# Kernel tuning notes

Hardware: AMD Instinct MI355X
Metric: run time of the kernel (lower is better)

Reference implementation:

```python
import jax, jax.numpy as jnp
import numpy as np

N_NODES = 100000
N_EDGES = 1600000
IN_DIM, HID, OUT_DIM = 256, 128, 64


def _glorot(key, shape):
    lim = float(np.sqrt(6.0 / (shape[0] + shape[1])))
    return jax.random.uniform(key, shape, jnp.float32, -lim, lim)


def setup_inputs() -> dict:
    key = jax.random.key(0)
    ks = jax.random.split(key, 8)
    x = jax.random.normal(ks[0], (N_NODES, IN_DIM), jnp.float32)
    edge_index = jax.random.randint(ks[1], (2, N_EDGES), 0, N_NODES, jnp.int64)
    return {
        "x": x,
        "edge_index": edge_index,
        "W1": _glorot(ks[2], (IN_DIM, HID)),
        "b1": jnp.zeros((HID,), jnp.float32),
        "W2": _glorot(ks[3], (HID, HID)),
        "b2": jnp.zeros((HID,), jnp.float32),
        "Wf1": _glorot(ks[4], (HID, HID)),
        "bf1": jnp.zeros((HID,), jnp.float32),
        "Wf2": _glorot(ks[5], (HID, OUT_DIM)),
        "bf2": jnp.zeros((OUT_DIM,), jnp.float32),
    }


def _gcn_conv(x, src, dst, W, b):
    # x: [N, Fin]; src/dst: [E+N] (self-loops already appended)
    n = x.shape[0]
    deg = jax.ops.segment_sum(jnp.ones_like(dst, dtype=x.dtype), dst, num_segments=n)
    dinv = jnp.where(deg > 0, jax.lax.rsqrt(deg), 0.0)
    norm = dinv[src] * dinv[dst]                      # [E+N]
    h = x @ W                                         # [N, Fout] transform first (PyG order)
    msg = h[src] * norm[:, None]                      # gather + scale
    return jax.ops.segment_sum(msg, dst, num_segments=n) + b


def reference(x, edge_index, W1, b1, W2, b2, Wf1, bf1, Wf2, bf2):
    n = x.shape[0]
    loops = jnp.arange(n, dtype=edge_index.dtype)
    src = jnp.concatenate([edge_index[0], loops])
    dst = jnp.concatenate([edge_index[1], loops])
    h = jax.nn.relu(_gcn_conv(x, src, dst, W1, b1))
    h = jax.nn.relu(_gcn_conv(h, src, dst, W2, b2))
    h = jax.nn.relu(h @ Wf1 + bf1)
    return h @ Wf2 + bf2
```

## Files before the change

kernel.cpp:

```cpp
#include <hip/hip_runtime.h>
#include <hip/hip_fp16.h>


typedef __attribute__((ext_vector_type(8))) short short8;
typedef __attribute__((ext_vector_type(4))) float f32x4;

constexpr int SLOT = 48;
constexpr int NBUK = 128;
constexpr int BCAP = 16000;
constexpr int NPB  = 782;

static __device__ __forceinline__ unsigned short f2bf(float f) {
    unsigned u = __float_as_uint(f);
    unsigned r = (u + 0x7fff + ((u >> 16) & 1)) >> 16;
    return (unsigned short)r;
}
static __device__ __forceinline__ float bf2f(unsigned short h) {
    return __uint_as_float(((unsigned)h) << 16);
}

static __device__ __forceinline__ void pack_one(
    const float* __restrict__ W, unsigned short* __restrict__ P,
    int Kd, int Nd, int idx)
{
    int k = idx / Nd, nn = idx % Nd;
    float w = W[idx];
    unsigned short hi = f2bf(w);
    unsigned short lo = f2bf(w - bf2f(hi));
    int k0 = k >> 5, kin = k & 31, bk = kin >> 3, i = kin & 7;
    int lane = (nn & 15) + (bk << 4);
    int cn = nn >> 4, NF = Nd >> 4;
    size_t base = (size_t)(k0 * NF + cn) * 1024;
    P[base + lane * 8 + i] = hi;
    P[base + 512 + lane * 8 + i] = lo;
}

__global__ void pack_all_k(const float* __restrict__ W1, const float* __restrict__ W2,
                           const float* __restrict__ Wf1, const float* __restrict__ Wf2,
                           unsigned short* __restrict__ W1p, unsigned short* __restrict__ W2p,
                           unsigned short* __restrict__ Wf1p, unsigned short* __restrict__ Wf2p,
                           int* __restrict__ gcur) {
    int gid = blockIdx.x * blockDim.x + threadIdx.x;
    const int n1 = 256 * 128, n2 = n1 + 128 * 128, n3 = n2 + 128 * 128, n4 = n3 + 128 * 64;
    if      (gid < n1) pack_one(W1,  W1p,  256, 128, gid);
    else if (gid < n2) pack_one(W2,  W2p,  128, 128, gid - n1);
    else if (gid < n3) pack_one(Wf1, Wf1p, 128, 128, gid - n2);
    else if (gid < n4) pack_one(Wf2, Wf2p, 128, 64,  gid - n3);
    else if (gid < n4 + NBUK) gcur[gid - n4] = 0;
}

template<int K, int N, bool SCALE, bool BIAS, bool RELU, bool HOUT>
static __device__ __forceinline__ void gemm_body(
    const float* __restrict__ A, const unsigned short* __restrict__ Bp,
    const float* __restrict__ bias, const float* __restrict__ dinv,
    void* __restrict__ Cv, int M, int bid)
{
    constexpr int NF = N / 16;
    constexpr int KS = K / 32;
    const int tid  = threadIdx.x;
    const int lane = tid & 63;
    const int wid  = tid >> 6;
    const int m16  = lane & 15;
    const int kg   = lane >> 4;
    const int rowB = bid * 128 + wid * 32;

    f32x4 acc[2][NF];
#pragma unroll
    for (int rm = 0; rm < 2; ++rm)
#pragma unroll
        for (int cn = 0; cn < NF; ++cn)
            acc[rm][cn] = (f32x4){0.f, 0.f, 0.f, 0.f};

    const short8* bp8 = (const short8*)Bp;

    for (int ks = 0; ks < KS; ++ks) {
        short8 ahi[2], alo[2];
#pragma unroll
        for (int rm = 0; rm < 2; ++rm) {
            int r = rowB + rm * 16 + m16;
            if (r >= M) r = M - 1;
            const float* ap = A + (size_t)r * K + ks * 32 + kg * 8;
            float4 a0 = *(const float4*)ap;
            float4 a1 = *(const float4*)(ap + 4);
            float av[8] = {a0.x, a0.y, a0.z, a0.w, a1.x, a1.y, a1.z, a1.w};
#pragma unroll
            for (int i = 0; i < 8; ++i) {
                unsigned short h = f2bf(av[i]);
                ahi[rm][i] = (short)h;
                alo[rm][i] = (short)f2bf(av[i] - bf2f(h));
            }
        }
#pragma unroll
        for (int cn = 0; cn < NF; ++cn) {
            size_t fb = (size_t)(ks * NF + cn) * 128 + lane;
            short8 bhi = bp8[fb];
            short8 blo = bp8[fb + 64];
#pragma unroll
            for (int rm = 0; rm < 2; ++rm) {
                acc[rm][cn] = __builtin_amdgcn_mfma_f32_16x16x32_bf16(ahi[rm], bhi, acc[rm][cn], 0, 0, 0);
                acc[rm][cn] = __builtin_amdgcn_mfma_f32_16x16x32_bf16(ahi[rm], blo, acc[rm][cn], 0, 0, 0);
                acc[rm][cn] = __builtin_amdgcn_mfma_f32_16x16x32_bf16(alo[rm], bhi, acc[rm][cn], 0, 0, 0);
            }
        }
    }
#pragma unroll
    for (int rm = 0; rm < 2; ++rm) {
#pragma unroll
        for (int r = 0; r < 4; ++r) {
            int row = rowB + rm * 16 + kg * 4 + r;
            if (row < M) {
                float sc = SCALE ? dinv[row] : 1.f;
#pragma unroll
                for (int cn = 0; cn < NF; ++cn) {
                    float v = acc[rm][cn][r];
                    if (SCALE) v *= sc;
                    if (BIAS)  v += bias[cn * 16 + m16];
                    if (RELU)  v = fmaxf(v, 0.f);
                    if (HOUT)
                        ((__half*)Cv)[(size_t)row * N + cn * 16 + m16] = __float2half(v);
                    else
                        ((float*)Cv)[(size_t)row * N + cn * 16 + m16] = v;
                }
            }
        }
    }
}

template<int K, int N, bool SCALE, bool BIAS, bool RELU, bool HOUT>
__global__ __launch_bounds__(256) void mgemm_k(
    const float* __restrict__ A, const unsigned short* __restrict__ Bp,
    const float* __restrict__ bias, const float* __restrict__ dinv,
    void* __restrict__ Cv, int M)
{
    gemm_body<K, N, SCALE, BIAS, RELU, HOUT>(A, Bp, bias, dinv, Cv, M, blockIdx.x);
}

__global__ __launch_bounds__(256) void mega1_k(
    const float* __restrict__ x, const unsigned short* __restrict__ W1p,
    __half* __restrict__ bufH, int M,
    const int* __restrict__ esrc, const int* __restrict__ edst,
    int2* __restrict__ bins, int* __restrict__ gcur, int E, int nGemm, int nChunk)
{
    __shared__ int hist[NBUK];
    __shared__ int bpos[NBUK];
    if ((int)blockIdx.x < nGemm) {
        gemm_body<256, 128, false, false, false, true>(x, W1p, nullptr, nullptr, bufH, M, blockIdx.x);
        return;
    }
    const int nb = gridDim.x - nGemm;
    for (int c = blockIdx.x - nGemm; c < nChunk; c += nb) {
        int base = c * 1024;
        if (threadIdx.x < NBUK) hist[threadIdx.x] = 0;
        __syncthreads();
        int d[4], s[4], bk[4], pl[4], ok[4];
#pragma unroll
        for (int i = 0; i < 4; ++i) {
            int e = base + threadIdx.x + i * 256;
            ok[i] = (e < E);
            d[i]  = ok[i] ? edst[e] : 0;
            s[i]  = ok[i] ? esrc[e] : 0;
            bk[i] = (int)((unsigned)d[i] / (unsigned)NPB);
        }
#pragma unroll
        for (int i = 0; i < 4; ++i)
            if (ok[i]) pl[i] = atomicAdd(&hist[bk[i]], 1);
        __syncthreads();
        if (threadIdx.x < NBUK) {
            int h = hist[threadIdx.x];
            bpos[threadIdx.x] = h ? atomicAdd(&gcur[threadIdx.x], h) : 0;
        }
        __syncthreads();
#pragma unroll
        for (int i = 0; i < 4; ++i)
            if (ok[i]) {
                int p = bpos[bk[i]] + pl[i];
                if (p < BCAP) bins[(size_t)bk[i] * BCAP + p] = make_int2(s[i], d[i]);
            }
        __syncthreads();
    }
}

__global__ __launch_bounds__(1024) void fill2_k(
    const int2* __restrict__ bins, const int* __restrict__ gcur,
    int* __restrict__ slot, float* __restrict__ dinv, int n)
{
    const int b = blockIdx.x;
    const int base = b * NPB;
    const int nn = min(NPB, n - base);
    if (nn <= 0) return;
    __shared__ int cnt[NPB];
    for (int i = threadIdx.x; i < nn; i += 1024) cnt[i] = 0;
    __syncthreads();
    int ec = gcur[b]; if (ec > BCAP) ec = BCAP;
    for (int i = threadIdx.x; i < ec; i += 1024) {
        int2 e = bins[(size_t)b * BCAP + i];
        int li = e.y - base;
        int p = atomicAdd(&cnt[li], 1);
        if (p < SLOT - 1) slot[(size_t)e.y * SLOT + 1 + p] = e.x;
    }
    __syncthreads();
    for (int i = threadIdx.x; i < nn; i += 1024) {
        int c = cnt[i];
        slot[(size_t)(base + i) * SLOT] = c;
        dinv[base + i] = 1.0f / sqrtf((float)(c + 1));
    }
}

struct alignas(16) H8 { __half2 h[4]; };

template<bool SS>
__global__ __launch_bounds__(256) void agg_k(
    const H8* __restrict__ hs, const int* __restrict__ slot,
    const float* __restrict__ dinv, const float* __restrict__ bias,
    float* __restrict__ out, int n)
{
    int t    = blockIdx.x * blockDim.x + threadIdx.x;
    int node = t >> 4;
    int ln   = threadIdx.x & 15;
    if (node >= n) return;
    const int* row = slot + (size_t)node * SLOT;
    int cnt = row[0]; if (cnt > SLOT - 1) cnt = SLOT - 1;
    float dn = dinv[node];

    float acc[8];
    {
        H8 v = hs[(size_t)node * 16 + ln];
        float sf = SS ? dn : 1.f;
#pragma unroll
        for (int q = 0; q < 4; ++q) {
            float2 f = __half22float2(v.h[q]);
            acc[q * 2] = f.x * sf; acc[q * 2 + 1] = f.y * sf;
        }
    }
    int j = 0;
    for (; j + 4 <= cnt; j += 4) {
        int s0 = row[1 + j], s1 = row[2 + j], s2 = row[3 + j], s3 = row[4 + j];
        float w0 = 1.f, w1 = 1.f, w2 = 1.f, w3 = 1.f;
        if (SS) { w0 = dinv[s0]; w1 = dinv[s1]; w2 = dinv[s2]; w3 = dinv[s3]; }
        H8 v0 = hs[(size_t)s0 * 16 + ln];
        H8 v1 = hs[(size_t)s1 * 16 + ln];
        H8 v2 = hs[(size_t)s2 * 16 + ln];
        H8 v3 = hs[(size_t)s3 * 16 + ln];
#pragma unroll
        for (int q = 0; q < 4; ++q) {
            float2 f0 = __half22float2(v0.h[q]);
            float2 f1 = __half22float2(v1.h[q]);
            float2 f2 = __half22float2(v2.h[q]);
            float2 f3 = __half22float2(v3.h[q]);
            if (SS) {
                acc[q*2]   = fmaf(w0, f0.x, fmaf(w1, f1.x, fmaf(w2, f2.x, fmaf(w3, f3.x, acc[q*2]))));
                acc[q*2+1] = fmaf(w0, f0.y, fmaf(w1, f1.y, fmaf(w2, f2.y, fmaf(w3, f3.y, acc[q*2+1]))));
            } else {
                acc[q*2]     += (f0.x + f1.x) + (f2.x + f3.x);
                acc[q*2 + 1] += (f0.y + f1.y) + (f2.y + f3.y);
            }
        }
    }
    for (; j < cnt; ++j) {
        int s = row[1 + j];
        float w = SS ? dinv[s] : 1.f;
        H8 v = hs[(size_t)s * 16 + ln];
#pragma unroll
        for (int q = 0; q < 4; ++q) {
            float2 f = __half22float2(v.h[q]);
            acc[q*2]     = fmaf(w, f.x, acc[q*2]);
            acc[q*2 + 1] = fmaf(w, f.y, acc[q*2 + 1]);
        }
    }
    float4 b0 = ((const float4*)bias)[ln * 2];
    float4 b1 = ((const float4*)bias)[ln * 2 + 1];
    float4 r0, r1;
    r0.x = fmaxf(fmaf(acc[0], dn, b0.x), 0.f);
    r0.y = fmaxf(fmaf(acc[1], dn, b0.y), 0.f);
    r0.z = fmaxf(fmaf(acc[2], dn, b0.z), 0.f);
    r0.w = fmaxf(fmaf(acc[3], dn, b0.w), 0.f);
    r1.x = fmaxf(fmaf(acc[4], dn, b1.x), 0.f);
    r1.y = fmaxf(fmaf(acc[5], dn, b1.y), 0.f);
    r1.z = fmaxf(fmaf(acc[6], dn, b1.z), 0.f);
    r1.w = fmaxf(fmaf(acc[7], dn, b1.w), 0.f);
    float4* op = (float4*)out;
    op[(size_t)node * 32 + ln * 2]     = r0;
    op[(size_t)node * 32 + ln * 2 + 1] = r1;
}

extern "C" void kernel_launch(void* const* d_in, const int* in_sizes, int n_in,
                              void* d_out, int out_size, void* d_ws, size_t ws_size,
                              hipStream_t stream) {
    const float* x    = (const float*)d_in[0];
    const int*   eidx = (const int*)d_in[1];
    const float* W1   = (const float*)d_in[2];
    const float* b1   = (const float*)d_in[3];
    const float* W2   = (const float*)d_in[4];
    const float* b2   = (const float*)d_in[5];
    const float* Wf1  = (const float*)d_in[6];
    const float* bf1  = (const float*)d_in[7];
    const float* Wf2  = (const float*)d_in[8];
    const float* bf2  = (const float*)d_in[9];
    float* out = (float*)d_out;

    const int IN = 256, HID = 128;
    const int n = in_sizes[0] / IN;
    const int E = in_sizes[1] / 2;
    const int* esrc = eidx;
    const int* edst = eidx + E;

    char* ws = (char*)d_ws;
    float*  bufB = (float*) (ws);
    int2*   bins = (int2*)  (ws);
    __half* bufH = (__half*)(ws + 51200000);
    int*    slot = (int*)   (ws + 76800000);
    float*  dinv = (float*) (ws + 96000000);
    int*    gcur = (int*)   (ws + 96400000);
    unsigned short* W1p  = (unsigned short*)(ws + 96500000);
    unsigned short* W2p  = (unsigned short*)(ws + 96631072);
    unsigned short* Wf1p = (unsigned short*)(ws + 96696608);
    unsigned short* Wf2p = (unsigned short*)(ws + 96762144);

    const int TB = 256;
    const int nPack  = 256*128 + 128*128 + 128*128 + 128*64 + NBUK;
    const int gGemm  = (n + 127) / 128;
    const int nChunk = (E + 1023) / 1024;
    const int gBin   = 384;
    const int gAgg   = (n * 16 + TB - 1) / TB;

    pack_all_k<<<(nPack + TB - 1) / TB, TB, 0, stream>>>(W1, W2, Wf1, Wf2,
                                                          W1p, W2p, Wf1p, Wf2p, gcur);
    mega1_k<<<gGemm + gBin, TB, 0, stream>>>(x, W1p, bufH, n, esrc, edst,
                                             bins, gcur, E, gGemm, nChunk);
    fill2_k<<<NBUK, 1024, 0, stream>>>(bins, gcur, slot, dinv, n);
    agg_k<true><<<gAgg, TB, 0, stream>>>((const H8*)bufH, slot, dinv, b1, bufB, n);
    mgemm_k<128, 128, true,  false, false, true ><<<gGemm, TB, 0, stream>>>(bufB, W2p, nullptr, dinv, bufH, n);
    agg_k<false><<<gAgg, TB, 0, stream>>>((const H8*)bufH, slot, dinv, b2, bufB, n);
    mgemm_k<128, 128, false, true,  true,  false><<<gGemm, TB, 0, stream>>>(bufB, Wf1p, bf1, nullptr, bufB, n);
    mgemm_k<128, 64,  false, true,  false, false><<<gGemm, TB, 0, stream>>>(bufB, Wf2p, bf2, nullptr, out, n);
}
```

Baseline: 446.2 us.

## Store intermediate activations in fp16 and restructure edge binning to one chunk per block

Aggregation outputs and the MLP intermediate activations are now stored as fp16 instead of fp32, and the GEMMs read half-precision A operands through a templated loader. This roughly halves the memory traffic between the aggregate and GEMM stages. The edge binning now uses 256 buckets with one 2048-edge chunk per block instead of a persistent grid-stride loop, and bin blocks are placed before the GEMM blocks in the fused launch. The cost is extra fp16 rounding on hidden activations, plus a different overlap between binning and the first GEMM.

```diff
diff --git a/kernel.cpp b/kernel.cpp
--- a/kernel.cpp
+++ b/kernel.cpp
@@ -5,10 +5,14 @@
 typedef __attribute__((ext_vector_type(8))) short short8;
 typedef __attribute__((ext_vector_type(4))) float f32x4;
 
-constexpr int SLOT = 48;
-constexpr int NBUK = 128;
-constexpr int BCAP = 16000;
-constexpr int NPB  = 782;
+constexpr int SLOT   = 48;
+constexpr int NBUK   = 256;
+constexpr int BCAP   = 8000;
+constexpr int NPB    = 391;
+constexpr int ECHUNK = 2048;
+constexpr int EPT    = 8;
+
+struct alignas(16) H8 { __half2 h[4]; };
 
 static __device__ __forceinline__ unsigned short f2bf(float f) {
     unsigned u = __float_as_uint(f);
@@ -17,6 +21,21 @@
 }
 static __device__ __forceinline__ float bf2f(unsigned short h) {
     return __uint_as_float(((unsigned)h) << 16);
+}
+
+static __device__ __forceinline__ void loadA8(const float* __restrict__ ap, float* av) {
+    float4 a0 = *(const float4*)ap;
+    float4 a1 = *(const float4*)(ap + 4);
+    av[0] = a0.x; av[1] = a0.y; av[2] = a0.z; av[3] = a0.w;
+    av[4] = a1.x; av[5] = a1.y; av[6] = a1.z; av[7] = a1.w;
+}
+static __device__ __forceinline__ void loadA8(const __half* __restrict__ ap, float* av) {
+    H8 hv = *(const H8*)ap;
+#pragma unroll
+    for (int q = 0; q < 4; ++q) {
+        float2 f = __half22float2(hv.h[q]);
+        av[2 * q] = f.x; av[2 * q + 1] = f.y;
+    }
 }
 
 static __device__ __forceinline__ void pack_one(
@@ -49,9 +68,9 @@
     else if (gid < n4 + NBUK) gcur[gid - n4] = 0;
 }
 
-template<int K, int N, bool SCALE, bool BIAS, bool RELU, bool HOUT>
+template<typename AT, int K, int N, bool SCALE, bool BIAS, bool RELU, bool HOUT>
 static __device__ __forceinline__ void gemm_body(
-    const float* __restrict__ A, const unsigned short* __restrict__ Bp,
+    const AT* __restrict__ A, const unsigned short* __restrict__ Bp,
     const float* __restrict__ bias, const float* __restrict__ dinv,
     void* __restrict__ Cv, int M, int bid)
 {
@@ -79,10 +98,8 @@
         for (int rm = 0; rm < 2; ++rm) {
             int r = rowB + rm * 16 + m16;
             if (r >= M) r = M - 1;
-            const float* ap = A + (size_t)r * K + ks * 32 + kg * 8;
-            float4 a0 = *(const float4*)ap;
-            float4 a1 = *(const float4*)(ap + 4);
-            float av[8] = {a0.x, a0.y, a0.z, a0.w, a1.x, a1.y, a1.z, a1.w};
+            float av[8];
+            loadA8(A + (size_t)r * K + ks * 32 + kg * 8, av);
 #pragma unroll
             for (int i = 0; i < 8; ++i) {
                 unsigned short h = f2bf(av[i]);
@@ -126,58 +143,55 @@
     }
 }
 
-template<int K, int N, bool SCALE, bool BIAS, bool RELU, bool HOUT>
+template<typename AT, int K, int N, bool SCALE, bool BIAS, bool RELU, bool HOUT>
 __global__ __launch_bounds__(256) void mgemm_k(
-    const float* __restrict__ A, const unsigned short* __restrict__ Bp,
+    const AT* __restrict__ A, const unsigned short* __restrict__ Bp,
     const float* __restrict__ bias, const float* __restrict__ dinv,
     void* __restrict__ Cv, int M)
 {
-    gemm_body<K, N, SCALE, BIAS, RELU, HOUT>(A, Bp, bias, dinv, Cv, M, blockIdx.x);
+    gemm_body<AT, K, N, SCALE, BIAS, RELU, HOUT>(A, Bp, bias, dinv, Cv, M, blockIdx.x);
 }
 
 __global__ __launch_bounds__(256) void mega1_k(
     const float* __restrict__ x, const unsigned short* __restrict__ W1p,
     __half* __restrict__ bufH, int M,
     const int* __restrict__ esrc, const int* __restrict__ edst,
-    int2* __restrict__ bins, int* __restrict__ gcur, int E, int nGemm, int nChunk)
+    int2* __restrict__ bins, int* __restrict__ gcur, int E, int nBin)
 {
     __shared__ int hist[NBUK];
     __shared__ int bpos[NBUK];
-    if ((int)blockIdx.x < nGemm) {
-        gemm_body<256, 128, false, false, false, true>(x, W1p, nullptr, nullptr, bufH, M, blockIdx.x);
+    if ((int)blockIdx.x >= nBin) {
+        gemm_body<float, 256, 128, false, false, false, true>(
+            x, W1p, nullptr, nullptr, bufH, M, blockIdx.x - nBin);
         return;
     }
-    const int nb = gridDim.x - nGemm;
-    for (int c = blockIdx.x - nGemm; c < nChunk; c += nb) {
-        int base = c * 1024;
-        if (threadIdx.x < NBUK) hist[threadIdx.x] = 0;
-        __syncthreads();
-        int d[4], s[4], bk[4], pl[4], ok[4];
-#pragma unroll
-        for (int i = 0; i < 4; ++i) {
-            int e = base + threadIdx.x + i * 256;
-            ok[i] = (e < E);
-            d[i]  = ok[i] ? edst[e] : 0;
-            s[i]  = ok[i] ? esrc[e] : 0;
-            bk[i] = (int)((unsigned)d[i] / (unsigned)NPB);
-        }
-#pragma unroll
-        for (int i = 0; i < 4; ++i)
-            if (ok[i]) pl[i] = atomicAdd(&hist[bk[i]], 1);
-        __syncthreads();
-        if (threadIdx.x < NBUK) {
-            int h = hist[threadIdx.x];
-            bpos[threadIdx.x] = h ? atomicAdd(&gcur[threadIdx.x], h) : 0;
-        }
-        __syncthreads();
-#pragma unroll
-        for (int i = 0; i < 4; ++i)
-            if (ok[i]) {
-                int p = bpos[bk[i]] + pl[i];
-                if (p < BCAP) bins[(size_t)bk[i] * BCAP + p] = make_int2(s[i], d[i]);
-            }
-        __syncthreads();
-    }
+    const int base = blockIdx.x * ECHUNK;
+    hist[threadIdx.x] = 0;
+    __syncthreads();
+    int d[EPT], s[EPT], bk[EPT], pl[EPT], ok[EPT];
+#pragma unroll
+    for (int i = 0; i < EPT; ++i) {
+        int e = base + threadIdx.x + i * 256;
+        ok[i] = (e < E);
+        d[i]  = ok[i] ? edst[e] : 0;
+        s[i]  = ok[i] ? esrc[e] : 0;
+        bk[i] = (int)((unsigned)d[i] / (unsigned)NPB);
+    }
+#pragma unroll
+    for (int i = 0; i < EPT; ++i)
+        if (ok[i]) pl[i] = atomicAdd(&hist[bk[i]], 1);
+    __syncthreads();
+    {
+        int h = hist[threadIdx.x];
+        bpos[threadIdx.x] = h ? atomicAdd(&gcur[threadIdx.x], h) : 0;
+    }
+    __syncthreads();
+#pragma unroll
+    for (int i = 0; i < EPT; ++i)
+        if (ok[i]) {
+            int p = bpos[bk[i]] + pl[i];
+            if (p < BCAP) bins[(size_t)bk[i] * BCAP + p] = make_int2(s[i], d[i]);
+        }
 }
 
 __global__ __launch_bounds__(1024) void fill2_k(
@@ -206,13 +220,11 @@
     }
 }
 
-struct alignas(16) H8 { __half2 h[4]; };
-
 template<bool SS>
 __global__ __launch_bounds__(256) void agg_k(
     const H8* __restrict__ hs, const int* __restrict__ slot,
     const float* __restrict__ dinv, const float* __restrict__ bias,
-    float* __restrict__ out, int n)
+    H8* __restrict__ out, int n)
 {
     int t    = blockIdx.x * blockDim.x + threadIdx.x;
     int node = t >> 4;
@@ -269,18 +281,16 @@
     }
     float4 b0 = ((const float4*)bias)[ln * 2];
     float4 b1 = ((const float4*)bias)[ln * 2 + 1];
-    float4 r0, r1;
-    r0.x = fmaxf(fmaf(acc[0], dn, b0.x), 0.f);
-    r0.y = fmaxf(fmaf(acc[1], dn, b0.y), 0.f);
-    r0.z = fmaxf(fmaf(acc[2], dn, b0.z), 0.f);
-    r0.w = fmaxf(fmaf(acc[3], dn, b0.w), 0.f);
-    r1.x = fmaxf(fmaf(acc[4], dn, b1.x), 0.f);
-    r1.y = fmaxf(fmaf(acc[5], dn, b1.y), 0.f);
-    r1.z = fmaxf(fmaf(acc[6], dn, b1.z), 0.f);
-    r1.w = fmaxf(fmaf(acc[7], dn, b1.w), 0.f);
-    float4* op = (float4*)out;
-    op[(size_t)node * 32 + ln * 2]     = r0;
-    op[(size_t)node * 32 + ln * 2 + 1] = r1;
+    H8 r;
+    r.h[0] = __floats2half2_rn(fmaxf(fmaf(acc[0], dn, b0.x), 0.f),
+                               fmaxf(fmaf(acc[1], dn, b0.y), 0.f));
+    r.h[1] = __floats2half2_rn(fmaxf(fmaf(acc[2], dn, b0.z), 0.f),
+                               fmaxf(fmaf(acc[3], dn, b0.w), 0.f));
+    r.h[2] = __floats2half2_rn(fmaxf(fmaf(acc[4], dn, b1.x), 0.f),
+                               fmaxf(fmaf(acc[5], dn, b1.y), 0.f));
+    r.h[3] = __floats2half2_rn(fmaxf(fmaf(acc[6], dn, b1.z), 0.f),
+                               fmaxf(fmaf(acc[7], dn, b1.w), 0.f));
+    out[(size_t)node * 16 + ln] = r;
 }
 
 extern "C" void kernel_launch(void* const* d_in, const int* in_sizes, int n_in,
@@ -305,32 +315,34 @@
     const int* edst = eidx + E;
 
     char* ws = (char*)d_ws;
-    float*  bufB = (float*) (ws);
-    int2*   bins = (int2*)  (ws);
-    __half* bufH = (__half*)(ws + 51200000);
-    int*    slot = (int*)   (ws + 76800000);
-    float*  dinv = (float*) (ws + 96000000);
-    int*    gcur = (int*)   (ws + 96400000);
-    unsigned short* W1p  = (unsigned short*)(ws + 96500000);
-    unsigned short* W2p  = (unsigned short*)(ws + 96631072);
-    unsigned short* Wf1p = (unsigned short*)(ws + 96696608);
-    unsigned short* Wf2p = (unsigned short*)(ws + 96762144);
+    __half* bufH1 = (__half*)(ws);
+    __half* bufH2 = (__half*)(ws + 25600000);
+    int2*   bins  = (int2*)  (ws + 25600000);
+    int*    slot  = (int*)   (ws + 51200000);
+    float*  dinv  = (float*) (ws + 70400000);
+    int*    gcur  = (int*)   (ws + 70800000);
+    unsigned short* W1p  = (unsigned short*)(ws + 70900000);
+    unsigned short* W2p  = (unsigned short*)(ws + 71040000);
+    unsigned short* Wf1p = (unsigned short*)(ws + 71110000);
+    unsigned short* Wf2p = (unsigned short*)(ws + 71180000);
 
     const int TB = 256;
-    const int nPack  = 256*128 + 128*128 + 128*128 + 128*64 + NBUK;
-    const int gGemm  = (n + 127) / 128;
-    const int nChunk = (E + 1023) / 1024;
-    const int gBin   = 384;
-    const int gAgg   = (n * 16 + TB - 1) / TB;
+    const int nPack = 256*128 + 128*128 + 128*128 + 128*64 + NBUK;
+    const int gGemm = (n + 127) / 128;
+    const int nBin  = (E + ECHUNK - 1) / ECHUNK;
+    const int gAgg  = (n * 16 + TB - 1) / TB;
 
     pack_all_k<<<(nPack + TB - 1) / TB, TB, 0, stream>>>(W1, W2, Wf1, Wf2,
                                                           W1p, W2p, Wf1p, Wf2p, gcur);
-    mega1_k<<<gGemm + gBin, TB, 0, stream>>>(x, W1p, bufH, n, esrc, edst,
-                                             bins, gcur, E, gGemm, nChunk);
+    mega1_k<<<nBin + gGemm, TB, 0, stream>>>(x, W1p, bufH1, n, esrc, edst,
+                                             bins, gcur, E, nBin);
     fill2_k<<<NBUK, 1024, 0, stream>>>(bins, gcur, slot, dinv, n);
-    agg_k<true><<<gAgg, TB, 0, stream>>>((const H8*)bufH, slot, dinv, b1, bufB, n);
-    mgemm_k<128, 128, true,  false, false, true ><<<gGemm, TB, 0, stream>>>(bufB, W2p, nullptr, dinv, bufH, n);
-    agg_k<false><<<gAgg, TB, 0, stream>>>((const H8*)bufH, slot, dinv, b2, bufB, n);
-    mgemm_k<128, 128, false, true,  true,  false><<<gGemm, TB, 0, stream>>>(bufB, Wf1p, bf1, nullptr, bufB, n);
-    mgemm_k<128, 64,  false, true,  false, false><<<gGemm, TB, 0, stream>>>(bufB, Wf2p, bf2, nullptr, out, n);
-}
+    agg_k<true><<<gAgg, TB, 0, stream>>>((const H8*)bufH1, slot, dinv, b1, (H8*)bufH2, n);
+    mgemm_k<__half, 128, 128, true,  false, false, true ><<<gGemm, TB, 0, stream>>>(
+        (const __half*)bufH2, W2p, nullptr, dinv, bufH1, n);
+    agg_k<false><<<gAgg, TB, 0, stream>>>((const H8*)bufH1, slot, dinv, b2, (H8*)bufH2, n);
+    mgemm_k<__half, 128, 128, false, true,  true,  true ><<<gGemm, TB, 0, stream>>>(
+        (const __half*)bufH2, Wf1p, bf1, nullptr, bufH1, n);
+    mgemm_k<__half, 128, 64,  false, true,  false, false><<<gGemm, TB, 0, stream>>>(
+        (const __half*)bufH1, Wf2p, bf2, nullptr, out, n);
+}
```

After: 427.7 us. 1.04x faster.
